# Kernel tuning notes

Hardware: AMD Instinct MI355X
Metric: run time of the kernel (lower is better)

The kernel has to match this reference:

```python
import jax, jax.numpy as jnp
import numpy as np

TEMPERATURE = 0.1
THR = 0.2
BORDER_RM = 2


def setup_inputs() -> dict:
    key = jax.random.key(0)
    k0, k1 = jax.random.split(key)
    N, L, S, C = 2, 4800, 4800, 256
    return {
        "feat_c0": jax.random.normal(k0, (N, L, C), dtype=jnp.float32),
        "feat_c1": jax.random.normal(k1, (N, S, C), dtype=jnp.float32),
        "h0c": 60, "w0c": 80, "h1c": 60, "w1c": 80,
    }


def _border_valid(h, w, bd):
    # Faithful to torch mask_border: only the FIRST `bd` rows/cols are masked
    # (the negative slices m[:, -bd:0] in the source are empty no-ops).
    vh = jnp.arange(h) >= bd
    vw = jnp.arange(w) >= bd
    return (vh[:, None] & vw[None, :]).reshape(-1)  # [h*w]


def reference(feat_c0, feat_c1, h0c, w0c, h1c, w1c):
    C = feat_c0.shape[-1]
    scale = 1.0 / (C ** 0.5)  # 'sqrt_feat_dim' feature normalizer
    f0 = feat_c0 * scale
    f1 = feat_c1 * scale

    # dual-softmax confidence matrix [N, L, S]
    sim = jnp.einsum("nlc,nsc->nls", f0, f1) / TEMPERATURE
    conf = jax.nn.softmax(sim, axis=1) * jax.nn.softmax(sim, axis=2)

    # threshold + border removal (no padding masks in data)
    mask = conf > THR
    valid0 = _border_valid(h0c, w0c, BORDER_RM)  # [L]
    valid1 = _border_valid(h1c, w1c, BORDER_RM)  # [S]
    mask = mask & valid0[None, :, None] & valid1[None, None, :]

    # mutual nearest neighbour filtering
    mask = mask & (conf == conf.max(axis=2, keepdims=True)) \
                & (conf == conf.max(axis=1, keepdims=True))

    # match extraction (JIT-friendly padded form):
    # j_ids[b, i] = column of the (unique) True in row i; match_mask marks valid rows.
    j_ids = jnp.argmax(mask, axis=2)               # [N, L] int
    match_mask = jnp.any(mask, axis=2)             # [N, L] bool
    mconf = jnp.take_along_axis(conf, j_ids[..., None], axis=2)[..., 0]
    mconf = jnp.where(match_mask, mconf, 0.0)      # [N, L]

    return conf, match_mask, j_ids, mconf
```

## Files before the change

### kernel.cpp

```cpp
#include <hip/hip_runtime.h>


#define Ncst 2
#define Lc 4800
#define Sc 4800
#define Cc 256
#define KA 512
#define KB 256
#define LP 4864
#define THRC 0.2f

typedef float f32x4 __attribute__((ext_vector_type(4)));
typedef _Float16 f16x8 __attribute__((ext_vector_type(8)));

#define AS1(p) ((__attribute__((address_space(1))) void*)(p))
#define AS3(p) ((__attribute__((address_space(3))) void*)(p))

__global__ __launch_bounds__(256) void convert_kernel(
    const float* __restrict__ f0, const float* __restrict__ f1,
    unsigned short* __restrict__ A2, unsigned short* __restrict__ B2,
    float* __restrict__ rs, float* __restrict__ cs, float* __restrict__ rcm)
{
    int idx = blockIdx.x * 256 + threadIdx.x;
    if (idx < Ncst * Lc) { rs[idx] = 0.f; cs[idx] = 0.f; rcm[idx] = 0.f; }
    if (idx >= Ncst * LP * (Cc / 8)) return;
    int k8  = idx & (Cc / 8 - 1);
    int row = (idx >> 5) % LP;
    int n   = idx / (LP * (Cc / 8));

    float av[8], bv[8];
    if (row < Lc) {
        const float4* pa = (const float4*)(f0 + ((size_t)n * Lc + row) * Cc + k8 * 8);
        float4 a0 = pa[0], a1 = pa[1];
        av[0]=a0.x; av[1]=a0.y; av[2]=a0.z; av[3]=a0.w;
        av[4]=a1.x; av[5]=a1.y; av[6]=a1.z; av[7]=a1.w;
        const float4* pb = (const float4*)(f1 + ((size_t)n * Sc + row) * Cc + k8 * 8);
        float4 b0 = pb[0], b1 = pb[1];
        bv[0]=b0.x; bv[1]=b0.y; bv[2]=b0.z; bv[3]=b0.w;
        bv[4]=b1.x; bv[5]=b1.y; bv[6]=b1.z; bv[7]=b1.w;
    } else {
        for (int i = 0; i < 8; ++i) { av[i] = 0.f; bv[i] = 0.f; }
    }

    _Float16 ahi[8], alo[8], bhi[8];
#pragma unroll
    for (int i = 0; i < 8; ++i) {
        _Float16 h = (_Float16)av[i];
        ahi[i] = h;
        alo[i] = (_Float16)(av[i] - (float)h);
        bhi[i] = (_Float16)bv[i];
    }
    size_t abase = ((size_t)n * LP + row) * KA + k8 * 8;
    size_t bbase = ((size_t)n * LP + row) * KB + k8 * 8;
    *(uint4*)&A2[abase]       = *(uint4*)ahi;
    *(uint4*)&A2[abase + 256] = *(uint4*)alo;
    *(uint4*)&B2[bbase]       = *(uint4*)bhi;
}

template <int PASS>
__global__ __launch_bounds__(256, 3) void gemm_kernel(
    const unsigned short* __restrict__ A2, const unsigned short* __restrict__ B2,
    float* __restrict__ out, float* __restrict__ rs, float* __restrict__ cs,
    int* __restrict__ rcm)
{
    __shared__ __attribute__((aligned(16))) unsigned short lds[2][1536 * 8];

    int flat = blockIdx.x + 38 * blockIdx.y + 1444 * blockIdx.z;
    int m    = (flat & 7) * 361 + (flat >> 3);
    const int tn = m % 38;
    const int tm = (m / 38) % 38;
    const int n  = m / 1444;

    const int tid  = threadIdx.x;
    const int wave = tid >> 6;
    const int lane = tid & 63;
    const int wm   = wave >> 1;
    const int wn   = wave & 1;
    const int ml   = lane & 15;
    const int kq   = lane >> 4;

    const unsigned short* Ab = A2 + ((size_t)n * LP + (size_t)tm * 128) * KA;
    const unsigned short* Bb = B2 + ((size_t)n * LP + (size_t)tn * 128) * KB;

    const unsigned short* gsrc[6];
    int gdst[6];
#pragma unroll
    for (int c = 0; c < 6; ++c) {
        int reg = c >> 1;
        int s   = (c & 1) * 256 + tid;
        int row = s >> 2;
        int q   = (s & 3) ^ ((row >> 1) & 3);
        if (reg == 0)      gsrc[c] = Ab + (size_t)row * KA + q * 8;
        else if (reg == 1) gsrc[c] = Ab + (size_t)row * KA + 256 + q * 8;
        else               gsrc[c] = Bb + (size_t)row * KB + q * 8;
        gdst[c] = (reg * 512 + s) * 8;
    }

    int aoff[4], boff[4];
#pragma unroll
    for (int i = 0; i < 4; ++i) {
        int ar = wm * 64 + i * 16 + ml;
        aoff[i] = (ar * 4 + (kq ^ ((ar >> 1) & 3))) * 8;
        int br = wn * 64 + i * 16 + ml;
        boff[i] = (br * 4 + (kq ^ ((br >> 1) & 3))) * 8;
    }

#define STAGE(bb, tt) do { _Pragma("unroll") for (int c_ = 0; c_ < 6; ++c_) \
    __builtin_amdgcn_global_load_lds(AS1(gsrc[c_] + (tt) * 32), AS3(&lds[bb][gdst[c_]]), 16, 0, 0); } while (0)

    f32x4 acc[4][4] = {};

    STAGE(0, 0);
    __syncthreads();

#pragma unroll
    for (int t = 0; t < 8; ++t) {
        const int b = t & 1;
        if (t < 7) STAGE(b ^ 1, t + 1);
        f16x8 ah[4], al[4], bf_[4];
#pragma unroll
        for (int i = 0; i < 4; ++i) {
            ah[i]  = *(const f16x8*)&lds[b][aoff[i]];
            al[i]  = *(const f16x8*)&lds[b][4096 + aoff[i]];
            bf_[i] = *(const f16x8*)&lds[b][8192 + boff[i]];
        }
#pragma unroll
        for (int i = 0; i < 4; ++i)
#pragma unroll
            for (int j = 0; j < 4; ++j) {
                acc[i][j] = __builtin_amdgcn_mfma_f32_16x16x32_f16(ah[i], bf_[j], acc[i][j], 0, 0, 0);
                acc[i][j] = __builtin_amdgcn_mfma_f32_16x16x32_f16(al[i], bf_[j], acc[i][j], 0, 0, 0);
            }
        __syncthreads();
    }
#undef STAGE

    const float alpha = 5.0f / 128.0f;

    if constexpr (PASS == 0) {
#pragma unroll
        for (int i = 0; i < 4; ++i)
#pragma unroll
            for (int r = 0; r < 4; ++r) {
                int gl = tm * 128 + wm * 64 + i * 16 + kq * 4 + r;
                bool rok = gl < Lc;
#pragma unroll
                for (int j = 0; j < 4; ++j) {
                    int gs = tn * 128 + wn * 64 + j * 16 + ml;
                    bool ok = rok && (gs < Sc);
                    acc[i][j][r] = ok ? __expf(acc[i][j][r] * alpha) : 0.f;
                }
            }
#pragma unroll
        for (int i = 0; i < 4; ++i)
#pragma unroll
            for (int r = 0; r < 4; ++r) {
                float rp = acc[i][0][r] + acc[i][1][r] + acc[i][2][r] + acc[i][3][r];
                rp += __shfl_xor(rp, 1);
                rp += __shfl_xor(rp, 2);
                rp += __shfl_xor(rp, 4);
                rp += __shfl_xor(rp, 8);
                int gl = tm * 128 + wm * 64 + i * 16 + kq * 4 + r;
                if (ml == 0 && gl < Lc) atomicAdd(&rs[(size_t)n * Lc + gl], rp);
            }
#pragma unroll
        for (int j = 0; j < 4; ++j) {
            float cp = 0.f;
#pragma unroll
            for (int i = 0; i < 4; ++i)
#pragma unroll
                for (int r = 0; r < 4; ++r) cp += acc[i][j][r];
            cp += __shfl_xor(cp, 16);
            cp += __shfl_xor(cp, 32);
            int gs = tn * 128 + wn * 64 + j * 16 + ml;
            if (kq == 0 && gs < Sc) atomicAdd(&cs[(size_t)n * Sc + gs], cp);
        }
    } else {
        float cin[4];
#pragma unroll
        for (int j = 0; j < 4; ++j) {
            int gs = tn * 128 + wn * 64 + j * 16 + ml;
            cin[j] = (gs < Sc) ? 1.0f / cs[(size_t)n * Sc + gs] : 0.f;
        }
#pragma unroll
        for (int i = 0; i < 4; ++i)
#pragma unroll
            for (int r = 0; r < 4; ++r) {
                int gl = tm * 128 + wm * 64 + i * 16 + kq * 4 + r;
                bool rok = gl < Lc;
                float ri = rok ? 1.0f / rs[(size_t)n * Lc + gl] : 0.f;
                float rmax = 0.f;
#pragma unroll
                for (int j = 0; j < 4; ++j) {
                    int gs = tn * 128 + wn * 64 + j * 16 + ml;
                    bool ok = rok && (gs < Sc);
                    float ev = __expf(acc[i][j][r] * alpha);
                    float c  = ev * ev * ri * cin[j];
                    if (!ok) c = 0.f;
                    if (ok) __builtin_nontemporal_store(c, &out[((size_t)n * Lc + gl) * Sc + gs]);
                    rmax = fmaxf(rmax, c);
                }
                rmax = fmaxf(rmax, __shfl_xor(rmax, 1));
                rmax = fmaxf(rmax, __shfl_xor(rmax, 2));
                rmax = fmaxf(rmax, __shfl_xor(rmax, 4));
                rmax = fmaxf(rmax, __shfl_xor(rmax, 8));
                if (ml == 0 && rok)
                    atomicMax(&rcm[(size_t)n * Lc + gl], __float_as_int(rmax));
            }
    }
}

__global__ __launch_bounds__(256) void finalize_kernel(
    const float* __restrict__ conf, const float* __restrict__ rcm,
    const int* __restrict__ h0p, const int* __restrict__ w0p,
    const int* __restrict__ h1p, const int* __restrict__ w1p,
    float* __restrict__ out_match, float* __restrict__ out_j, float* __restrict__ out_mconf)
{
    int i = blockIdx.x * 256 + threadIdx.x;
    if (i >= Ncst * Lc) return;
    int n = i / Lc, l = i % Lc;
    float mm = rcm[i];
    float fm = 0.f, fj = 0.f, fc = 0.f;
    if (mm > THRC) {
        int w0 = *w0p, w1 = *w1p;
        if ((l / w0) >= 2 && (l % w0) >= 2) {
            const float* rowp = conf + ((size_t)n * Lc + l) * Sc;
            for (int s = 0; s < Sc; ++s) {
                float c = rowp[s];
                if (c == mm && (s / w1) >= 2 && (s % w1) >= 2) {
                    bool ismax = true;
                    const float* colp = conf + (size_t)n * Lc * Sc + s;
                    for (int lp = 0; lp < Lc; ++lp) {
                        if (colp[(size_t)lp * Sc] > c) { ismax = false; break; }
                    }
                    if (ismax) { fm = 1.f; fj = (float)s; fc = c; break; }
                }
            }
        }
    }
    out_match[i] = fm; out_j[i] = fj; out_mconf[i] = fc;
}

extern "C" void kernel_launch(void* const* d_in, const int* in_sizes, int n_in,
                              void* d_out, int out_size, void* d_ws, size_t ws_size,
                              hipStream_t stream) {
    const float* f0 = (const float*)d_in[0];
    const float* f1 = (const float*)d_in[1];
    const int* h0p = (const int*)d_in[2];
    const int* w0p = (const int*)d_in[3];
    const int* h1p = (const int*)d_in[4];
    const int* w1p = (const int*)d_in[5];

    char* ws = (char*)d_ws;
    unsigned short* A2 = (unsigned short*)ws;
    unsigned short* B2 = (unsigned short*)(ws + 9961472);
    float* rs  = (float*)(ws + 14942208);
    float* cs  = (float*)(ws + 14980608);
    float* rcm = (float*)(ws + 15019008);

    float* conf      = (float*)d_out;
    float* out_match = conf + (size_t)Ncst * Lc * Sc;
    float* out_j     = out_match + Ncst * Lc;
    float* out_mconf = out_j + Ncst * Lc;

    convert_kernel<<<(Ncst * LP * (Cc / 8) + 255) / 256, 256, 0, stream>>>(
        f0, f1, A2, B2, rs, cs, rcm);

    dim3 gg(38, 38, Ncst);
    gemm_kernel<0><<<gg, 256, 0, stream>>>(A2, B2, nullptr, rs, cs, nullptr);
    gemm_kernel<1><<<gg, 256, 0, stream>>>(A2, B2, conf, rs, cs, (int*)rcm);

    finalize_kernel<<<(Ncst * Lc + 255) / 256, 256, 0, stream>>>(
        conf, rcm, h0p, w0p, h1p, w1p, out_match, out_j, out_mconf);
}
```

Measured before the change: 340.2 us.

## Replace second GEMM pass with exp store and streaming normalization kernel

Instead of recomputing the split-fp16 GEMM in a second pass, the single GEMM pass writes exp(sim) to the output buffer and accumulates row and column sums. A new inverse kernel and a row-wise streaming conf kernel then read that buffer back, apply the row and column normalizations, and compute each row max without atomics. This removes a full GEMM's compute but adds an extra read and write of the 184 MB conf matrix, so the outcome depends on whether the kernel is compute- or bandwidth-bound.

Result: faster. 317.0 us (-6.8%).

```diff
diff --git a/kernel.cpp b/kernel.cpp
--- a/kernel.cpp
+++ b/kernel.cpp
@@ -19,10 +19,10 @@
 __global__ __launch_bounds__(256) void convert_kernel(
     const float* __restrict__ f0, const float* __restrict__ f1,
     unsigned short* __restrict__ A2, unsigned short* __restrict__ B2,
-    float* __restrict__ rs, float* __restrict__ cs, float* __restrict__ rcm)
+    float* __restrict__ rs, float* __restrict__ cs)
 {
     int idx = blockIdx.x * 256 + threadIdx.x;
-    if (idx < Ncst * Lc) { rs[idx] = 0.f; cs[idx] = 0.f; rcm[idx] = 0.f; }
+    if (idx < Ncst * Lc) { rs[idx] = 0.f; cs[idx] = 0.f; }
     if (idx >= Ncst * LP * (Cc / 8)) return;
     int k8  = idx & (Cc / 8 - 1);
     int row = (idx >> 5) % LP;
@@ -57,11 +57,10 @@
     *(uint4*)&B2[bbase]       = *(uint4*)bhi;
 }
 
-template <int PASS>
+template <int DUMMY>
 __global__ __launch_bounds__(256, 3) void gemm_kernel(
     const unsigned short* __restrict__ A2, const unsigned short* __restrict__ B2,
-    float* __restrict__ out, float* __restrict__ rs, float* __restrict__ cs,
-    int* __restrict__ rcm)
+    float* __restrict__ eout, float* __restrict__ rs, float* __restrict__ cs)
 {
     __shared__ __attribute__((aligned(16))) unsigned short lds[2][1536 * 8];
 
@@ -136,78 +135,81 @@
 #undef STAGE
 
     const float alpha = 5.0f / 128.0f;
-
-    if constexpr (PASS == 0) {
+#pragma unroll
+    for (int i = 0; i < 4; ++i) {
+#pragma unroll
+        for (int r = 0; r < 4; ++r) {
+            int gl = tm * 128 + wm * 64 + i * 16 + kq * 4 + r;
+            bool rok = gl < Lc;
+#pragma unroll
+            for (int j = 0; j < 4; ++j) {
+                int gs = tn * 128 + wn * 64 + j * 16 + ml;
+                bool ok = rok && (gs < Sc);
+                float ev = ok ? __expf(acc[i][j][r] * alpha) : 0.f;
+                acc[i][j][r] = ev;
+                if (ok) eout[((size_t)n * Lc + gl) * Sc + gs] = ev;
+            }
+        }
+    }
+#pragma unroll
+    for (int i = 0; i < 4; ++i) {
+#pragma unroll
+        for (int r = 0; r < 4; ++r) {
+            float rp = acc[i][0][r] + acc[i][1][r] + acc[i][2][r] + acc[i][3][r];
+            rp += __shfl_xor(rp, 1);
+            rp += __shfl_xor(rp, 2);
+            rp += __shfl_xor(rp, 4);
+            rp += __shfl_xor(rp, 8);
+            int gl = tm * 128 + wm * 64 + i * 16 + kq * 4 + r;
+            if (ml == 0 && gl < Lc) atomicAdd(&rs[(size_t)n * Lc + gl], rp);
+        }
+    }
+#pragma unroll
+    for (int j = 0; j < 4; ++j) {
+        float cp = 0.f;
 #pragma unroll
         for (int i = 0; i < 4; ++i)
 #pragma unroll
-            for (int r = 0; r < 4; ++r) {
-                int gl = tm * 128 + wm * 64 + i * 16 + kq * 4 + r;
-                bool rok = gl < Lc;
-#pragma unroll
-                for (int j = 0; j < 4; ++j) {
-                    int gs = tn * 128 + wn * 64 + j * 16 + ml;
-                    bool ok = rok && (gs < Sc);
-                    acc[i][j][r] = ok ? __expf(acc[i][j][r] * alpha) : 0.f;
-                }
-            }
-#pragma unroll
-        for (int i = 0; i < 4; ++i)
-#pragma unroll
-            for (int r = 0; r < 4; ++r) {
-                float rp = acc[i][0][r] + acc[i][1][r] + acc[i][2][r] + acc[i][3][r];
-                rp += __shfl_xor(rp, 1);
-                rp += __shfl_xor(rp, 2);
-                rp += __shfl_xor(rp, 4);
-                rp += __shfl_xor(rp, 8);
-                int gl = tm * 128 + wm * 64 + i * 16 + kq * 4 + r;
-                if (ml == 0 && gl < Lc) atomicAdd(&rs[(size_t)n * Lc + gl], rp);
-            }
-#pragma unroll
-        for (int j = 0; j < 4; ++j) {
-            float cp = 0.f;
-#pragma unroll
-            for (int i = 0; i < 4; ++i)
-#pragma unroll
-                for (int r = 0; r < 4; ++r) cp += acc[i][j][r];
-            cp += __shfl_xor(cp, 16);
-            cp += __shfl_xor(cp, 32);
-            int gs = tn * 128 + wn * 64 + j * 16 + ml;
-            if (kq == 0 && gs < Sc) atomicAdd(&cs[(size_t)n * Sc + gs], cp);
-        }
-    } else {
-        float cin[4];
-#pragma unroll
-        for (int j = 0; j < 4; ++j) {
-            int gs = tn * 128 + wn * 64 + j * 16 + ml;
-            cin[j] = (gs < Sc) ? 1.0f / cs[(size_t)n * Sc + gs] : 0.f;
-        }
-#pragma unroll
-        for (int i = 0; i < 4; ++i)
-#pragma unroll
-            for (int r = 0; r < 4; ++r) {
-                int gl = tm * 128 + wm * 64 + i * 16 + kq * 4 + r;
-                bool rok = gl < Lc;
-                float ri = rok ? 1.0f / rs[(size_t)n * Lc + gl] : 0.f;
-                float rmax = 0.f;
-#pragma unroll
-                for (int j = 0; j < 4; ++j) {
-                    int gs = tn * 128 + wn * 64 + j * 16 + ml;
-                    bool ok = rok && (gs < Sc);
-                    float ev = __expf(acc[i][j][r] * alpha);
-                    float c  = ev * ev * ri * cin[j];
-                    if (!ok) c = 0.f;
-                    if (ok) __builtin_nontemporal_store(c, &out[((size_t)n * Lc + gl) * Sc + gs]);
-                    rmax = fmaxf(rmax, c);
-                }
-                rmax = fmaxf(rmax, __shfl_xor(rmax, 1));
-                rmax = fmaxf(rmax, __shfl_xor(rmax, 2));
-                rmax = fmaxf(rmax, __shfl_xor(rmax, 4));
-                rmax = fmaxf(rmax, __shfl_xor(rmax, 8));
-                if (ml == 0 && rok)
-                    atomicMax(&rcm[(size_t)n * Lc + gl], __float_as_int(rmax));
-            }
-    }
+            for (int r = 0; r < 4; ++r) cp += acc[i][j][r];
+        cp += __shfl_xor(cp, 16);
+        cp += __shfl_xor(cp, 32);
+        int gs = tn * 128 + wn * 64 + j * 16 + ml;
+        if (kq == 0 && gs < Sc) atomicAdd(&cs[(size_t)n * Sc + gs], cp);
+    }
+}
+
+__global__ __launch_bounds__(256) void inv_kernel(
+    const float* __restrict__ cs, float* __restrict__ csinv)
+{
+    int i = blockIdx.x * 256 + threadIdx.x;
+    if (i < Ncst * Lc) csinv[i] = 1.0f / cs[i];
+}
+
+__global__ __launch_bounds__(256) void conf_kernel(
+    float* __restrict__ confio,
+    const float* __restrict__ rs, const float* __restrict__ csinv,
+    float* __restrict__ rcm)
+{
+    __shared__ float sw[4];
+    int b = blockIdx.x;
+    int n = b / Lc;
+    f32x4* row = (f32x4*)(confio + (size_t)b * Sc);
+    const f32x4* civ = (const f32x4*)(csinv + (size_t)n * Sc);
+    int tid = threadIdx.x;
+    float riv = 1.0f / rs[b];
+    float lmax = 0.f;
+    for (int v = tid; v < Sc / 4; v += 256) {
+        f32x4 e4 = row[v];
+        f32x4 c4 = civ[v];
+        f32x4 o  = e4 * e4 * riv * c4;
+        __builtin_nontemporal_store(o, &row[v]);
+        lmax = fmaxf(lmax, fmaxf(fmaxf(o.x, o.y), fmaxf(o.z, o.w)));
+    }
+#pragma unroll
+    for (int off = 1; off < 64; off <<= 1) lmax = fmaxf(lmax, __shfl_xor(lmax, off));
+    if ((tid & 63) == 0) sw[tid >> 6] = lmax;
+    __syncthreads();
+    if (tid == 0) rcm[b] = fmaxf(fmaxf(sw[0], sw[1]), fmaxf(sw[2], sw[3]));
 }
 
 __global__ __launch_bounds__(256) void finalize_kernel(
@@ -254,9 +256,10 @@
     char* ws = (char*)d_ws;
     unsigned short* A2 = (unsigned short*)ws;
     unsigned short* B2 = (unsigned short*)(ws + 9961472);
-    float* rs  = (float*)(ws + 14942208);
-    float* cs  = (float*)(ws + 14980608);
-    float* rcm = (float*)(ws + 15019008);
+    float* rs    = (float*)(ws + 14942208);
+    float* cs    = (float*)(ws + 14980608);
+    float* csinv = (float*)(ws + 15019008);
+    float* rcm   = (float*)(ws + 15057408);
 
     float* conf      = (float*)d_out;
     float* out_match = conf + (size_t)Ncst * Lc * Sc;
@@ -264,11 +267,14 @@
     float* out_mconf = out_j + Ncst * Lc;
 
     convert_kernel<<<(Ncst * LP * (Cc / 8) + 255) / 256, 256, 0, stream>>>(
-        f0, f1, A2, B2, rs, cs, rcm);
+        f0, f1, A2, B2, rs, cs);
 
     dim3 gg(38, 38, Ncst);
-    gemm_kernel<0><<<gg, 256, 0, stream>>>(A2, B2, nullptr, rs, cs, nullptr);
-    gemm_kernel<1><<<gg, 256, 0, stream>>>(A2, B2, conf, rs, cs, (int*)rcm);
+    gemm_kernel<0><<<gg, 256, 0, stream>>>(A2, B2, conf, rs, cs);
+
+    inv_kernel<<<(Ncst * Lc + 255) / 256, 256, 0, stream>>>(cs, csinv);
+
+    conf_kernel<<<Ncst * Lc, 256, 0, stream>>>(conf, rs, csinv, rcm);
 
     finalize_kernel<<<(Ncst * Lc + 255) / 256, 256, 0, stream>>>(
         conf, rcm, h0p, w0p, h1p, w1p, out_match, out_j, out_mconf);
```
